# Optimization experiments

Measured on AMD Instinct MI355X. Metric: run time of the kernel, lower is better.

## Reference

```python
import jax, jax.numpy as jnp
import numpy as np

EPS = 1e-10


def setup_inputs() -> dict:
    key = jax.random.key(0)
    ks = jax.random.split(key, 8)
    b, s, m, r, n = 2, 2048, 1024, 64, 16
    u = jax.random.normal(ks[0], (b, s, m), dtype=jnp.float32)
    delta = jax.random.normal(ks[1], (b, s, r), dtype=jnp.float32)
    dt_proj_w = jax.random.normal(ks[2], (m, r), dtype=jnp.float32) * 0.02
    dt_proj_b = jax.random.normal(ks[3], (m,), dtype=jnp.float32) * 0.02
    # A_log ~ Uniform(-3, -1) as in nn.init.uniform_(self.A_log, -3.0, -1.0)
    A_log = jax.random.uniform(ks[4], (n, m), dtype=jnp.float32, minval=-3.0, maxval=-1.0)
    D_skip = jnp.ones((m,), dtype=jnp.float32)
    # xavier_uniform with gain=0.1 on [n, m]
    bound = 0.1 * np.sqrt(6.0 / (n + m))
    B_proj_w = jax.random.uniform(ks[5], (n, m), dtype=jnp.float32, minval=-bound, maxval=bound)
    C_proj_w = jax.random.uniform(ks[6], (n, m), dtype=jnp.float32, minval=-bound, maxval=bound)
    return {"u": u, "delta": delta, "dt_proj_w": dt_proj_w, "dt_proj_b": dt_proj_b,
            "A_log": A_log, "D_skip": D_skip, "B_proj_w": B_proj_w, "C_proj_w": C_proj_w}


def reference(u, delta, dt_proj_w, dt_proj_b, A_log, D_skip, B_proj_w, C_proj_w):
    # u: [b, s, m]; delta: [b, s, r]
    dt = jax.nn.softplus(jnp.einsum('bsr,mr->bsm', delta, dt_proj_w) + dt_proj_b)
    dt = jnp.clip(dt, 1e-6, 10.0)                      # [b, s, m]
    A = jnp.clip(-jnp.exp(A_log), -10.0, -1e-6)        # [n, m]
    B = jnp.einsum('bsm,nm->bsn', u, B_proj_w)         # [b, s, n]
    C = jnp.einsum('bsm,nm->bsn', u, C_proj_w)         # [b, s, n]

    # associative-scan path (seq_len > 256), math as in _associative_scan:
    # h_t = exp(cumsum_t log(dA)) * cumsum_t (dB_u / dA)
    dA = jnp.exp(dt[:, :, None, :] * A[None, None])    # [b, s, n, m]
    dA_c = jnp.clip(dA, EPS, None)
    dBu = dt[:, :, None, :] * B[..., None] * u[:, :, None, :]  # [b, s, n, m]
    A_cum = jnp.exp(jnp.cumsum(jnp.log(dA_c), axis=1))
    h = A_cum * jnp.cumsum(dBu / dA_c, axis=1)          # [b, s, n, m]
    y = jnp.einsum('bsnm,bsn->bsm', h, C)               # contract state dim

    out = y + u * D_skip
    out = jnp.clip(out, -10000.0, 10000.0)
    bad = jnp.any(~jnp.isfinite(out))
    return jnp.where(bad, jnp.zeros_like(u), out)
```

## Files before the change

kernel.cpp:

```cpp
#include <hip/hip_runtime.h>
#include <hip/hip_bf16.h>
#include <math.h>

#define B_ 2
#define S_ 2048
#define M_ 1024
#define R_ 64
#define N_ 16
#define NC 64
#define CH (S_/NC)

#define DT_OFF  0
#define P_OFF   4194304
#define H_OFF   6291456
#define BWT_OFF 8388608
#define CWT_OFF 8404992
#define PB_OFF  8421376
#define PC_OFF  8552448

__global__ __launch_bounds__(256) void k_dt(const float* __restrict__ delta,
                                            const float* __restrict__ Wdt,
                                            const float* __restrict__ bdt,
                                            const float* __restrict__ Bw,
                                            const float* __restrict__ Cw,
                                            float* __restrict__ dt,
                                            float* __restrict__ BwT,
                                            float* __restrict__ CwT) {
    int bid = blockIdx.y * 4 + blockIdx.x;
    if (threadIdx.x < 8) {
        int idx = bid * 8 + threadIdx.x;
        int mt = idx >> 4, nt = idx & 15;
        BwT[idx] = Bw[nt * M_ + mt];
        CwT[idx] = Cw[nt * M_ + mt];
    }
    int m    = blockIdx.x * 256 + threadIdx.x;
    int row0 = blockIdx.y * 8;
    float w[R_];
    const float4* W4 = reinterpret_cast<const float4*>(Wdt + (size_t)m * R_);
#pragma unroll
    for (int i = 0; i < R_ / 4; ++i) {
        float4 v = W4[i];
        w[4*i] = v.x; w[4*i+1] = v.y; w[4*i+2] = v.z; w[4*i+3] = v.w;
    }
    float bias = bdt[m];
#pragma unroll 1
    for (int r = 0; r < 8; ++r) {
        int bs = row0 + r;
        const float* dr = delta + (size_t)bs * R_;
        float acc = bias;
#pragma unroll
        for (int k = 0; k < R_; ++k) acc = fmaf(dr[k], w[k], acc);
        float sp = fmaxf(acc, 0.f) + log1pf(expf(-fabsf(acc)));
        sp = fminf(fmaxf(sp, 1e-6f), 10.0f);
        dt[(size_t)bs * M_ + m] = sp;
    }
}

__global__ __launch_bounds__(256) void k_bc_partial(const float* __restrict__ u,
                                                    const float* __restrict__ BwT,
                                                    const float* __restrict__ CwT,
                                                    float* __restrict__ pB,
                                                    float* __restrict__ pC) {
    __shared__ float uLds[16 * 516];
    int r0 = blockIdx.x * 16;
    int k0 = blockIdx.y * 512;
    for (int i = threadIdx.x; i < 2048; i += 256) {
        int r = i >> 7, kq = i & 127;
        float4 v = *reinterpret_cast<const float4*>(&u[(size_t)(r0 + r) * M_ + k0 + kq * 4]);
        *reinterpret_cast<float4*>(&uLds[r * 516 + kq * 4]) = v;
    }
    __syncthreads();
    int r = threadIdx.x >> 4, n = threadIdx.x & 15;
    const float4* u4 = reinterpret_cast<const float4*>(uLds + r * 516);
    float accB = 0.f, accC = 0.f;
#pragma unroll 4
    for (int k4 = 0; k4 < 128; ++k4) {
        float4 uv = u4[k4];
        int kb = k0 + k4 * 4;
        accB = fmaf(uv.x, BwT[(kb+0)*16 + n], accB);
        accB = fmaf(uv.y, BwT[(kb+1)*16 + n], accB);
        accB = fmaf(uv.z, BwT[(kb+2)*16 + n], accB);
        accB = fmaf(uv.w, BwT[(kb+3)*16 + n], accB);
        accC = fmaf(uv.x, CwT[(kb+0)*16 + n], accC);
        accC = fmaf(uv.y, CwT[(kb+1)*16 + n], accC);
        accC = fmaf(uv.z, CwT[(kb+2)*16 + n], accC);
        accC = fmaf(uv.w, CwT[(kb+3)*16 + n], accC);
    }
    size_t o = (size_t)blockIdx.y * 65536 + (size_t)(r0 + r) * 16 + n;
    pB[o] = accB;
    pC[o] = accC;
}

__global__ __launch_bounds__(256) void k_pass1(const float* __restrict__ dt,
                                               const float* __restrict__ u,
                                               const float* __restrict__ pB,
                                               const float* __restrict__ A_log,
                                               float* __restrict__ P,
                                               float* __restrict__ H) {
    __shared__ float ldsDt[CH * 64], ldsU[CH * 64], ldsB[CH * 16];
    int m0 = blockIdx.x * 64, c = blockIdx.y, b = blockIdx.z;
    int s0 = c * CH;
    int tid = threadIdx.x;
    for (int i = tid; i < 512; i += 256) {
        int s = i >> 4, mq = (i & 15) * 4;
        size_t off = ((size_t)(b * S_ + s0 + s)) * M_ + m0 + mq;
        *reinterpret_cast<float4*>(&ldsDt[s * 64 + mq]) = *reinterpret_cast<const float4*>(&dt[off]);
        *reinterpret_cast<float4*>(&ldsU [s * 64 + mq]) = *reinterpret_cast<const float4*>(&u[off]);
    }
    {
        size_t base = (size_t)(b * S_ + s0) * N_;
        for (int i = tid; i < CH * 16; i += 256)
            ldsB[i] = pB[base + i] + pB[65536 + base + i];
    }
    __syncthreads();
    int lane = tid & 63, wave = tid >> 6;
    int ml = wave * 16 + (lane & 15);
    int m  = m0 + ml;
    int n0 = (lane >> 4) * 4;
    float Aa[4], h[4] = {0,0,0,0}, g[4] = {1.f,1.f,1.f,1.f};
#pragma unroll
    for (int j = 0; j < 4; ++j) {
        float a = -expf(A_log[(size_t)(n0 + j) * M_ + m]);
        Aa[j] = fminf(fmaxf(a, -10.f), -1e-6f);
    }
    for (int s = 0; s < CH; ++s) {
        float dtv = ldsDt[s * 64 + ml];
        float uv  = ldsU [s * 64 + ml];
        float du  = dtv * uv;
        float4 bv = *reinterpret_cast<const float4*>(&ldsB[s * 16 + n0]);
        float bb[4] = {bv.x, bv.y, bv.z, bv.w};
#pragma unroll
        for (int j = 0; j < 4; ++j) {
            float ea = __expf(dtv * Aa[j]);
            h[j] = fmaf(ea, h[j], g[j] * (du * bb[j]));
            g[j] *= ea;
        }
    }
#pragma unroll
    for (int j = 0; j < 4; ++j) {
        size_t o = ((size_t)(b * 16 + n0 + j) * NC + c) * M_ + m;
        P[o] = g[j];
        H[o] = h[j];
    }
}

__global__ __launch_bounds__(64) void k_pass2(float* __restrict__ P,
                                              float* __restrict__ H) {
    int idx = blockIdx.x * 64 + threadIdx.x;
    int m = idx & (M_ - 1);
    int n = (idx >> 10) & 15;
    int b = idx >> 14;
    size_t base = ((size_t)(b * 16 + n) * NC) * M_ + m;
    float grun = 1.f, hrun = 0.f;
#pragma unroll 1
    for (int c0 = 0; c0 < NC; c0 += 8) {
        float pv[8], hv[8];
#pragma unroll
        for (int t = 0; t < 8; ++t) {
            pv[t] = P[base + (size_t)(c0 + t) * M_];
            hv[t] = H[base + (size_t)(c0 + t) * M_];
        }
#pragma unroll
        for (int t = 0; t < 8; ++t) {
            P[base + (size_t)(c0 + t) * M_] = grun;
            H[base + (size_t)(c0 + t) * M_] = hrun;
            hrun = fmaf(pv[t], hrun, grun * hv[t]);
            grun *= pv[t];
        }
    }
}

__global__ __launch_bounds__(256) void k_pass3(const float* __restrict__ dt,
                                               const float* __restrict__ u,
                                               const float* __restrict__ pB,
                                               const float* __restrict__ pC,
                                               const float* __restrict__ A_log,
                                               const float* __restrict__ Dskip,
                                               const float* __restrict__ Pinit,
                                               const float* __restrict__ Hinit,
                                               float* __restrict__ out) {
    __shared__ float ldsDt[CH * 64], ldsU[CH * 64], ldsB[CH * 16], ldsC[CH * 16];
    int m0 = blockIdx.x * 64, c = blockIdx.y, b = blockIdx.z;
    int s0 = c * CH;
    int tid = threadIdx.x;
    for (int i = tid; i < 512; i += 256) {
        int s = i >> 4, mq = (i & 15) * 4;
        size_t off = ((size_t)(b * S_ + s0 + s)) * M_ + m0 + mq;
        *reinterpret_cast<float4*>(&ldsDt[s * 64 + mq]) = *reinterpret_cast<const float4*>(&dt[off]);
        *reinterpret_cast<float4*>(&ldsU [s * 64 + mq]) = *reinterpret_cast<const float4*>(&u[off]);
    }
    {
        size_t base = (size_t)(b * S_ + s0) * N_;
        for (int i = tid; i < CH * 16; i += 256) {
            ldsB[i] = pB[base + i] + pB[65536 + base + i];
            ldsC[i] = pC[base + i] + pC[65536 + base + i];
        }
    }
    __syncthreads();
    int lane = tid & 63, wave = tid >> 6;
    int ml = wave * 16 + (lane & 15);
    int m  = m0 + ml;
    int ng = lane >> 4, n0 = ng * 4;
    float Aa[4], h[4], g[4];
#pragma unroll
    for (int j = 0; j < 4; ++j) {
        float a = -expf(A_log[(size_t)(n0 + j) * M_ + m]);
        Aa[j] = fminf(fmaxf(a, -10.f), -1e-6f);
        size_t o = ((size_t)(b * 16 + n0 + j) * NC + c) * M_ + m;
        g[j] = Pinit[o];
        h[j] = Hinit[o];
    }
    float Dm = Dskip[m];
    for (int s = 0; s < CH; ++s) {
        float dtv = ldsDt[s * 64 + ml];
        float uv  = ldsU [s * 64 + ml];
        float du  = dtv * uv;
        float4 bv = *reinterpret_cast<const float4*>(&ldsB[s * 16 + n0]);
        float4 cv = *reinterpret_cast<const float4*>(&ldsC[s * 16 + n0]);
        float bb[4] = {bv.x, bv.y, bv.z, bv.w};
        float cc[4] = {cv.x, cv.y, cv.z, cv.w};
        float y = 0.f;
#pragma unroll
        for (int j = 0; j < 4; ++j) {
            float ea = __expf(dtv * Aa[j]);
            h[j] = fmaf(ea, h[j], g[j] * (du * bb[j]));
            g[j] *= ea;
            y = fmaf(h[j], cc[j], y);
        }
        y += __shfl_xor(y, 16, 64);
        y += __shfl_xor(y, 32, 64);
        if (ng == 0) {
            float o = y + uv * Dm;
            o = fminf(fmaxf(o, -10000.f), 10000.f);
            out[((size_t)(b * S_ + s0 + s)) * M_ + m] = o;
        }
    }
}

extern "C" void kernel_launch(void* const* d_in, const int* in_sizes, int n_in,
                              void* d_out, int out_size, void* d_ws, size_t ws_size,
                              hipStream_t stream) {
    const float* u     = (const float*)d_in[0];
    const float* delta = (const float*)d_in[1];
    const float* Wdt   = (const float*)d_in[2];
    const float* bdt   = (const float*)d_in[3];
    const float* A_log = (const float*)d_in[4];
    const float* Dski  = (const float*)d_in[5];
    const float* Bw    = (const float*)d_in[6];
    const float* Cw    = (const float*)d_in[7];
    float* out = (float*)d_out;
    float* ws  = (float*)d_ws;

    float* dt  = ws + DT_OFF;
    float* P   = ws + P_OFF;
    float* H   = ws + H_OFF;
    float* BwT = ws + BWT_OFF;
    float* CwT = ws + CWT_OFF;
    float* pB  = ws + PB_OFF;
    float* pC  = ws + PC_OFF;

    k_dt<<<dim3(4, 512), 256, 0, stream>>>(delta, Wdt, bdt, Bw, Cw, dt, BwT, CwT);
    k_bc_partial<<<dim3(256, 2), 256, 0, stream>>>(u, BwT, CwT, pB, pC);
    k_pass1<<<dim3(16, NC, B_), 256, 0, stream>>>(dt, u, pB, A_log, P, H);
    k_pass2<<<512, 64, 0, stream>>>(P, H);
    k_pass3<<<dim3(16, NC, B_), 256, 0, stream>>>(dt, u, pB, pC, A_log, Dski, P, H, out);
}
```

Before: 106.8 us.

## Fuse all five stages into one cooperative kernel with grid syncs

Result: no change. 106.9 us (+0.1%).

```diff
diff --git a/kernel.cpp b/kernel.cpp
--- a/kernel.cpp
+++ b/kernel.cpp
@@ -1,6 +1,8 @@
 #include <hip/hip_runtime.h>
-#include <hip/hip_bf16.h>
+#include <hip/hip_cooperative_groups.h>
 #include <math.h>
+
+namespace cg = cooperative_groups;
 
 #define B_ 2
 #define S_ 2048
@@ -17,6 +19,247 @@
 #define CWT_OFF 8404992
 #define PB_OFF  8421376
 #define PC_OFF  8552448
+
+__global__ __launch_bounds__(256, 8) void k_mega(
+    const float* __restrict__ u, const float* __restrict__ delta,
+    const float* __restrict__ Wdt, const float* __restrict__ bdt,
+    const float* __restrict__ A_log, const float* __restrict__ Dskip,
+    const float* __restrict__ Bw, const float* __restrict__ Cw,
+    float* __restrict__ P, float* __restrict__ H,
+    float* __restrict__ Bp, float* __restrict__ Cp,
+    float* __restrict__ out)
+{
+    cg::grid_group grid = cg::this_grid();
+    __shared__ float lds[5120];
+    const int tid = threadIdx.x;
+    const int bid = blockIdx.x;
+    const int b   = bid >> 10;
+    const int c   = (bid >> 4) & 63;
+    const int m0  = (bid & 15) << 6;
+    const int s0  = c << 5;
+
+    if (bid < 512) {
+        const int msp = tid >> 4;
+        const int nn  = tid & 15;
+        const float4* wB4 = reinterpret_cast<const float4*>(Bw + (size_t)nn * M_ + msp * 64);
+        const float4* wC4 = reinterpret_cast<const float4*>(Cw + (size_t)nn * M_ + msp * 64);
+        for (int half = 0; half < 2; ++half) {
+            const int rowBase = bid * 8 + half * 4;
+            for (int i = tid; i < 1024; i += 256) {
+                int r = i >> 8, kq = i & 255;
+                *reinterpret_cast<float4*>(&lds[r * 1024 + kq * 4]) =
+                    *reinterpret_cast<const float4*>(&u[(size_t)(rowBase + r) * M_ + kq * 4]);
+            }
+            __syncthreads();
+            float accB[4] = {0.f,0.f,0.f,0.f}, accC[4] = {0.f,0.f,0.f,0.f};
+#pragma unroll 1
+            for (int k4 = 0; k4 < 16; ++k4) {
+                float4 wb = wB4[k4], wc = wC4[k4];
+#pragma unroll
+                for (int r = 0; r < 4; ++r) {
+                    float4 uv = *reinterpret_cast<const float4*>(&lds[r * 1024 + msp * 64 + k4 * 4]);
+                    accB[r] = fmaf(uv.x, wb.x, accB[r]);
+                    accB[r] = fmaf(uv.y, wb.y, accB[r]);
+                    accB[r] = fmaf(uv.z, wb.z, accB[r]);
+                    accB[r] = fmaf(uv.w, wb.w, accB[r]);
+                    accC[r] = fmaf(uv.x, wc.x, accC[r]);
+                    accC[r] = fmaf(uv.y, wc.y, accC[r]);
+                    accC[r] = fmaf(uv.z, wc.z, accC[r]);
+                    accC[r] = fmaf(uv.w, wc.w, accC[r]);
+                }
+            }
+#pragma unroll
+            for (int r = 0; r < 4; ++r) {
+                accB[r] += __shfl_xor(accB[r], 16, 64);
+                accB[r] += __shfl_xor(accB[r], 32, 64);
+                accC[r] += __shfl_xor(accC[r], 16, 64);
+                accC[r] += __shfl_xor(accC[r], 32, 64);
+            }
+            __syncthreads();
+            {
+                const int w  = tid >> 6;
+                const int ln = tid & 63;
+                if (ln < 16) {
+#pragma unroll
+                    for (int r = 0; r < 4; ++r) {
+                        lds[4096 + (w * 4 + r) * 16 + ln]       = accB[r];
+                        lds[4096 + 256 + (w * 4 + r) * 16 + ln] = accC[r];
+                    }
+                }
+            }
+            __syncthreads();
+            if (tid < 64) {
+                int r = tid >> 4, n2 = tid & 15;
+                float sB = 0.f, sC = 0.f;
+#pragma unroll
+                for (int w2 = 0; w2 < 4; ++w2) {
+                    sB += lds[4096 + (w2 * 4 + r) * 16 + n2];
+                    sC += lds[4096 + 256 + (w2 * 4 + r) * 16 + n2];
+                }
+                Bp[(size_t)(rowBase + r) * N_ + n2] = sB;
+                Cp[(size_t)(rowBase + r) * N_ + n2] = sC;
+            }
+            __syncthreads();
+        }
+    }
+
+    for (int i = tid; i < 512; i += 256) {
+        int s = i >> 4, kq = (i & 15) * 4;
+        *reinterpret_cast<float4*>(&lds[2048 + s * 64 + kq]) =
+            *reinterpret_cast<const float4*>(&delta[(size_t)(b * S_ + s0 + s) * R_ + kq]);
+    }
+    __syncthreads();
+    {
+        const int mlA = tid & 63;
+        const int sg  = tid >> 6;
+        const int mA  = m0 + mlA;
+        float bias = bdt[mA];
+        float acc[8];
+#pragma unroll
+        for (int i = 0; i < 8; ++i) acc[i] = bias;
+        const float4* W4 = reinterpret_cast<const float4*>(Wdt + (size_t)mA * R_);
+#pragma unroll 1
+        for (int kb = 0; kb < 8; ++kb) {
+            float4 w0 = W4[kb * 2], w1 = W4[kb * 2 + 1];
+#pragma unroll
+            for (int i = 0; i < 8; ++i) {
+                const float* dr = &lds[2048 + (sg * 8 + i) * 64 + kb * 8];
+                float4 d0 = *reinterpret_cast<const float4*>(dr);
+                float4 d1 = *reinterpret_cast<const float4*>(dr + 4);
+                acc[i] = fmaf(d0.x, w0.x, acc[i]);
+                acc[i] = fmaf(d0.y, w0.y, acc[i]);
+                acc[i] = fmaf(d0.z, w0.z, acc[i]);
+                acc[i] = fmaf(d0.w, w0.w, acc[i]);
+                acc[i] = fmaf(d1.x, w1.x, acc[i]);
+                acc[i] = fmaf(d1.y, w1.y, acc[i]);
+                acc[i] = fmaf(d1.z, w1.z, acc[i]);
+                acc[i] = fmaf(d1.w, w1.w, acc[i]);
+            }
+        }
+#pragma unroll
+        for (int i = 0; i < 8; ++i) {
+            float a2 = acc[i];
+            float sp = fmaxf(a2, 0.f) + log1pf(expf(-fabsf(a2)));
+            sp = fminf(fmaxf(sp, 1e-6f), 10.0f);
+            lds[(sg * 8 + i) * 64 + mlA] = sp;
+        }
+    }
+    __syncthreads();
+    for (int i = tid; i < 512; i += 256) {
+        int s = i >> 4, mq = (i & 15) * 4;
+        *reinterpret_cast<float4*>(&lds[2048 + s * 64 + mq]) =
+            *reinterpret_cast<const float4*>(&u[((size_t)(b * S_ + s0 + s)) * M_ + m0 + mq]);
+    }
+
+    const int lane = tid & 63;
+    const int wv   = tid >> 6;
+    const int ml   = wv * 16 + (lane & 15);
+    const int m    = m0 + ml;
+    const int ng   = lane >> 4;
+    const int n0   = ng * 4;
+    float Aa[4];
+#pragma unroll
+    for (int j = 0; j < 4; ++j) {
+        float a2 = -expf(A_log[(size_t)(n0 + j) * M_ + m]);
+        Aa[j] = fminf(fmaxf(a2, -10.f), -1e-6f);
+    }
+    const float Dm = Dskip[m];
+
+    grid.sync();
+
+    {
+        const size_t baseBC = (size_t)(b * S_ + s0) * N_;
+        if (tid < 128) {
+            *reinterpret_cast<float4*>(&lds[4096 + tid * 4]) =
+                *reinterpret_cast<const float4*>(&Bp[baseBC + tid * 4]);
+        } else {
+            *reinterpret_cast<float4*>(&lds[4608 + (tid - 128) * 4]) =
+                *reinterpret_cast<const float4*>(&Cp[baseBC + (tid - 128) * 4]);
+        }
+    }
+    __syncthreads();
+
+    float h[4] = {0.f,0.f,0.f,0.f}, g[4] = {1.f,1.f,1.f,1.f};
+    for (int s = 0; s < CH; ++s) {
+        float dtv = lds[s * 64 + ml];
+        float uv  = lds[2048 + s * 64 + ml];
+        float du  = dtv * uv;
+        float4 bv = *reinterpret_cast<const float4*>(&lds[4096 + s * 16 + n0]);
+        float bb[4] = {bv.x, bv.y, bv.z, bv.w};
+#pragma unroll
+        for (int j = 0; j < 4; ++j) {
+            float ea = __expf(dtv * Aa[j]);
+            h[j] = fmaf(ea, h[j], g[j] * (du * bb[j]));
+            g[j] *= ea;
+        }
+    }
+#pragma unroll
+    for (int j = 0; j < 4; ++j) {
+        size_t o = ((size_t)((b * N_ + n0 + j) * NC + c)) * M_ + m;
+        P[o] = g[j];
+        H[o] = h[j];
+    }
+
+    grid.sync();
+
+    if (bid < 128) {
+        const int idx = bid * 256 + tid;
+        const int mm  = idx & (M_ - 1);
+        const int nn2 = (idx >> 10) & 15;
+        const int bb2 = idx >> 14;
+        const size_t base2 = ((size_t)(bb2 * N_ + nn2) * NC) * M_ + mm;
+        float grun = 1.f, hrun = 0.f;
+#pragma unroll 1
+        for (int c0 = 0; c0 < NC; c0 += 8) {
+            float pv[8], hv[8];
+#pragma unroll
+            for (int t = 0; t < 8; ++t) {
+                pv[t] = P[base2 + (size_t)(c0 + t) * M_];
+                hv[t] = H[base2 + (size_t)(c0 + t) * M_];
+            }
+#pragma unroll
+            for (int t = 0; t < 8; ++t) {
+                P[base2 + (size_t)(c0 + t) * M_] = grun;
+                H[base2 + (size_t)(c0 + t) * M_] = hrun;
+                hrun = fmaf(pv[t], hrun, grun * hv[t]);
+                grun *= pv[t];
+            }
+        }
+    }
+
+    grid.sync();
+
+#pragma unroll
+    for (int j = 0; j < 4; ++j) {
+        size_t o = ((size_t)((b * N_ + n0 + j) * NC + c)) * M_ + m;
+        g[j] = P[o];
+        h[j] = H[o];
+    }
+    for (int s = 0; s < CH; ++s) {
+        float dtv = lds[s * 64 + ml];
+        float uv  = lds[2048 + s * 64 + ml];
+        float du  = dtv * uv;
+        float4 bv = *reinterpret_cast<const float4*>(&lds[4096 + s * 16 + n0]);
+        float4 cv = *reinterpret_cast<const float4*>(&lds[4608 + s * 16 + n0]);
+        float bb[4] = {bv.x, bv.y, bv.z, bv.w};
+        float cc[4] = {cv.x, cv.y, cv.z, cv.w};
+        float y = 0.f;
+#pragma unroll
+        for (int j = 0; j < 4; ++j) {
+            float ea = __expf(dtv * Aa[j]);
+            h[j] = fmaf(ea, h[j], g[j] * (du * bb[j]));
+            g[j] *= ea;
+            y = fmaf(h[j], cc[j], y);
+        }
+        y += __shfl_xor(y, 16, 64);
+        y += __shfl_xor(y, 32, 64);
+        if (ng == 0) {
+            float o2 = y + uv * Dm;
+            o2 = fminf(fmaxf(o2, -10000.f), 10000.f);
+            out[((size_t)(b * S_ + s0 + s)) * M_ + m] = o2;
+        }
+    }
+}
 
 __global__ __launch_bounds__(256) void k_dt(const float* __restrict__ delta,
                                             const float* __restrict__ Wdt,
@@ -259,6 +502,19 @@
     float* pB  = ws + PB_OFF;
     float* pC  = ws + PC_OFF;
 
+    int maxBlk = 0;
+    hipError_t qerr = hipOccupancyMaxActiveBlocksPerMultiprocessor(
+        &maxBlk, reinterpret_cast<const void*>(k_mega), 256, 0);
+    if (qerr == hipSuccess && maxBlk >= 8) {
+        void* args[] = {(void*)&u, (void*)&delta, (void*)&Wdt, (void*)&bdt,
+                        (void*)&A_log, (void*)&Dski, (void*)&Bw, (void*)&Cw,
+                        (void*)&P, (void*)&H, (void*)&pB, (void*)&pC, (void*)&out};
+        hipError_t lerr = hipLaunchCooperativeKernel(
+            reinterpret_cast<const void*>(k_mega), dim3(2048), dim3(256),
+            args, 0, stream);
+        if (lerr == hipSuccess) return;
+    }
+
     k_dt<<<dim3(4, 512), 256, 0, stream>>>(delta, Wdt, bdt, Bw, Cw, dt, BwT, CwT);
     k_bc_partial<<<dim3(256, 2), 256, 0, stream>>>(u, BwT, CwT, pB, pC);
     k_pass1<<<dim3(16, NC, B_), 256, 0, stream>>>(dt, u, pB, A_log, P, H);
```

## Merge front kernels, drop chunk-prefix kernel, recompute prefix in pass3

Applied to the files above, without the earlier changes.

Result: slower. 154.4 us (+44.6%).

```diff
diff --git a/kernel.cpp b/kernel.cpp
--- a/kernel.cpp
+++ b/kernel.cpp
@@ -1,5 +1,4 @@
 #include <hip/hip_runtime.h>
-#include <hip/hip_bf16.h>
 #include <math.h>
 
 #define B_ 2
@@ -7,101 +6,89 @@
 #define M_ 1024
 #define R_ 64
 #define N_ 16
-#define NC 64
-#define CH (S_/NC)
+#define NC 32
+#define CH 64
 
 #define DT_OFF  0
-#define P_OFF   4194304
-#define H_OFF   6291456
-#define BWT_OFF 8388608
-#define CWT_OFF 8404992
-#define PB_OFF  8421376
-#define PC_OFF  8552448
-
-__global__ __launch_bounds__(256) void k_dt(const float* __restrict__ delta,
-                                            const float* __restrict__ Wdt,
-                                            const float* __restrict__ bdt,
-                                            const float* __restrict__ Bw,
-                                            const float* __restrict__ Cw,
-                                            float* __restrict__ dt,
-                                            float* __restrict__ BwT,
-                                            float* __restrict__ CwT) {
-    int bid = blockIdx.y * 4 + blockIdx.x;
-    if (threadIdx.x < 8) {
-        int idx = bid * 8 + threadIdx.x;
-        int mt = idx >> 4, nt = idx & 15;
-        BwT[idx] = Bw[nt * M_ + mt];
-        CwT[idx] = Cw[nt * M_ + mt];
-    }
-    int m    = blockIdx.x * 256 + threadIdx.x;
-    int row0 = blockIdx.y * 8;
-    float w[R_];
-    const float4* W4 = reinterpret_cast<const float4*>(Wdt + (size_t)m * R_);
-#pragma unroll
-    for (int i = 0; i < R_ / 4; ++i) {
-        float4 v = W4[i];
-        w[4*i] = v.x; w[4*i+1] = v.y; w[4*i+2] = v.z; w[4*i+3] = v.w;
-    }
-    float bias = bdt[m];
+#define AGG_OFF 4194304
+#define PB_OFF  6291456
+#define PC_OFF  6422528
+
+__global__ __launch_bounds__(256) void k_front(
+    const float* __restrict__ u, const float* __restrict__ delta,
+    const float* __restrict__ Wdt, const float* __restrict__ bdt,
+    const float* __restrict__ Bw, const float* __restrict__ Cw,
+    float* __restrict__ dt, float* __restrict__ pB, float* __restrict__ pC)
+{
+    __shared__ float uLds[16 * 516];
+    const int bid = blockIdx.x;
+    const int tid = threadIdx.x;
+
+    if (bid < 512) {
+        const int r0 = (bid >> 1) * 16;
+        const int k0 = (bid & 1) * 512;
+        for (int i = tid; i < 2048; i += 256) {
+            int r = i >> 7, kq = i & 127;
+            *reinterpret_cast<float4*>(&uLds[r * 516 + kq * 4]) =
+                *reinterpret_cast<const float4*>(&u[(size_t)(r0 + r) * M_ + k0 + kq * 4]);
+        }
+        __syncthreads();
+        const int r = tid >> 4, n = tid & 15;
+        const float4* u4  = reinterpret_cast<const float4*>(uLds + r * 516);
+        const float4* wB4 = reinterpret_cast<const float4*>(Bw + (size_t)n * M_ + k0);
+        const float4* wC4 = reinterpret_cast<const float4*>(Cw + (size_t)n * M_ + k0);
+        float accB = 0.f, accC = 0.f;
+#pragma unroll 4
+        for (int k4 = 0; k4 < 128; ++k4) {
+            float4 uv = u4[k4], wb = wB4[k4], wc = wC4[k4];
+            accB = fmaf(uv.x, wb.x, accB);
+            accB = fmaf(uv.y, wb.y, accB);
+            accB = fmaf(uv.z, wb.z, accB);
+            accB = fmaf(uv.w, wb.w, accB);
+            accC = fmaf(uv.x, wc.x, accC);
+            accC = fmaf(uv.y, wc.y, accC);
+            accC = fmaf(uv.z, wc.z, accC);
+            accC = fmaf(uv.w, wc.w, accC);
+        }
+        size_t o = (size_t)(bid & 1) * 65536 + (size_t)(r0 + r) * 16 + n;
+        pB[o] = accB;
+        pC[o] = accC;
+    } else {
+        const int bid2 = bid - 512;
+        const int m    = (bid2 & 3) * 256 + tid;
+        const int row0 = (bid2 >> 2) * 8;
+        float w[R_];
+        const float4* W4 = reinterpret_cast<const float4*>(Wdt + (size_t)m * R_);
+#pragma unroll
+        for (int i = 0; i < R_ / 4; ++i) {
+            float4 v = W4[i];
+            w[4*i] = v.x; w[4*i+1] = v.y; w[4*i+2] = v.z; w[4*i+3] = v.w;
+        }
+        float bias = bdt[m];
 #pragma unroll 1
-    for (int r = 0; r < 8; ++r) {
-        int bs = row0 + r;
-        const float* dr = delta + (size_t)bs * R_;
-        float acc = bias;
-#pragma unroll
-        for (int k = 0; k < R_; ++k) acc = fmaf(dr[k], w[k], acc);
-        float sp = fmaxf(acc, 0.f) + log1pf(expf(-fabsf(acc)));
-        sp = fminf(fmaxf(sp, 1e-6f), 10.0f);
-        dt[(size_t)bs * M_ + m] = sp;
-    }
-}
-
-__global__ __launch_bounds__(256) void k_bc_partial(const float* __restrict__ u,
-                                                    const float* __restrict__ BwT,
-                                                    const float* __restrict__ CwT,
-                                                    float* __restrict__ pB,
-                                                    float* __restrict__ pC) {
-    __shared__ float uLds[16 * 516];
-    int r0 = blockIdx.x * 16;
-    int k0 = blockIdx.y * 512;
-    for (int i = threadIdx.x; i < 2048; i += 256) {
-        int r = i >> 7, kq = i & 127;
-        float4 v = *reinterpret_cast<const float4*>(&u[(size_t)(r0 + r) * M_ + k0 + kq * 4]);
-        *reinterpret_cast<float4*>(&uLds[r * 516 + kq * 4]) = v;
-    }
-    __syncthreads();
-    int r = threadIdx.x >> 4, n = threadIdx.x & 15;
-    const float4* u4 = reinterpret_cast<const float4*>(uLds + r * 516);
-    float accB = 0.f, accC = 0.f;
-#pragma unroll 4
-    for (int k4 = 0; k4 < 128; ++k4) {
-        float4 uv = u4[k4];
-        int kb = k0 + k4 * 4;
-        accB = fmaf(uv.x, BwT[(kb+0)*16 + n], accB);
-        accB = fmaf(uv.y, BwT[(kb+1)*16 + n], accB);
-        accB = fmaf(uv.z, BwT[(kb+2)*16 + n], accB);
-        accB = fmaf(uv.w, BwT[(kb+3)*16 + n], accB);
-        accC = fmaf(uv.x, CwT[(kb+0)*16 + n], accC);
-        accC = fmaf(uv.y, CwT[(kb+1)*16 + n], accC);
-        accC = fmaf(uv.z, CwT[(kb+2)*16 + n], accC);
-        accC = fmaf(uv.w, CwT[(kb+3)*16 + n], accC);
-    }
-    size_t o = (size_t)blockIdx.y * 65536 + (size_t)(r0 + r) * 16 + n;
-    pB[o] = accB;
-    pC[o] = accC;
+        for (int r = 0; r < 8; ++r) {
+            int bs = row0 + r;
+            const float* dr = delta + (size_t)bs * R_;
+            float acc = bias;
+#pragma unroll
+            for (int k = 0; k < R_; ++k) acc = fmaf(dr[k], w[k], acc);
+            float sp = fmaxf(acc, 0.f) + log1pf(expf(-fabsf(acc)));
+            sp = fminf(fmaxf(sp, 1e-6f), 10.0f);
+            dt[(size_t)bs * M_ + m] = sp;
+        }
+    }
 }
 
 __global__ __launch_bounds__(256) void k_pass1(const float* __restrict__ dt,
                                                const float* __restrict__ u,
                                                const float* __restrict__ pB,
                                                const float* __restrict__ A_log,
-                                               float* __restrict__ P,
-                                               float* __restrict__ H) {
+                                               float* __restrict__ Agg) {
     __shared__ float ldsDt[CH * 64], ldsU[CH * 64], ldsB[CH * 16];
-    int m0 = blockIdx.x * 64, c = blockIdx.y, b = blockIdx.z;
-    int s0 = c * CH;
-    int tid = threadIdx.x;
-    for (int i = tid; i < 512; i += 256) {
+    const int m0 = blockIdx.x * 64, c = blockIdx.y, b = blockIdx.z;
+    const int s0 = c * CH;
+    const int tid = threadIdx.x;
+    for (int i = tid; i < 1024; i += 256) {
         int s = i >> 4, mq = (i & 15) * 4;
         size_t off = ((size_t)(b * S_ + s0 + s)) * M_ + m0 + mq;
         *reinterpret_cast<float4*>(&ldsDt[s * 64 + mq]) = *reinterpret_cast<const float4*>(&dt[off]);
@@ -113,10 +100,10 @@
             ldsB[i] = pB[base + i] + pB[65536 + base + i];
     }
     __syncthreads();
-    int lane = tid & 63, wave = tid >> 6;
-    int ml = wave * 16 + (lane & 15);
-    int m  = m0 + ml;
-    int n0 = (lane >> 4) * 4;
+    const int lane = tid & 63, wave = tid >> 6;
+    const int ml = wave * 16 + (lane & 15);
+    const int m  = m0 + ml;
+    const int n0 = (lane >> 4) * 4;
     float Aa[4], h[4] = {0,0,0,0}, g[4] = {1.f,1.f,1.f,1.f};
 #pragma unroll
     for (int j = 0; j < 4; ++j) {
@@ -136,38 +123,11 @@
             g[j] *= ea;
         }
     }
-#pragma unroll
-    for (int j = 0; j < 4; ++j) {
-        size_t o = ((size_t)(b * 16 + n0 + j) * NC + c) * M_ + m;
-        P[o] = g[j];
-        H[o] = h[j];
-    }
-}
-
-__global__ __launch_bounds__(64) void k_pass2(float* __restrict__ P,
-                                              float* __restrict__ H) {
-    int idx = blockIdx.x * 64 + threadIdx.x;
-    int m = idx & (M_ - 1);
-    int n = (idx >> 10) & 15;
-    int b = idx >> 14;
-    size_t base = ((size_t)(b * 16 + n) * NC) * M_ + m;
-    float grun = 1.f, hrun = 0.f;
-#pragma unroll 1
-    for (int c0 = 0; c0 < NC; c0 += 8) {
-        float pv[8], hv[8];
-#pragma unroll
-        for (int t = 0; t < 8; ++t) {
-            pv[t] = P[base + (size_t)(c0 + t) * M_];
-            hv[t] = H[base + (size_t)(c0 + t) * M_];
-        }
-#pragma unroll
-        for (int t = 0; t < 8; ++t) {
-            P[base + (size_t)(c0 + t) * M_] = grun;
-            H[base + (size_t)(c0 + t) * M_] = hrun;
-            hrun = fmaf(pv[t], hrun, grun * hv[t]);
-            grun *= pv[t];
-        }
-    }
+    size_t base = ((size_t)(b * NC + c) * 1024 + m) * 32 + n0 * 2;
+    float4 w0 = make_float4(g[0], h[0], g[1], h[1]);
+    float4 w1 = make_float4(g[2], h[2], g[3], h[3]);
+    *reinterpret_cast<float4*>(&Agg[base])     = w0;
+    *reinterpret_cast<float4*>(&Agg[base + 4]) = w1;
 }
 
 __global__ __launch_bounds__(256) void k_pass3(const float* __restrict__ dt,
@@ -176,14 +136,13 @@
                                                const float* __restrict__ pC,
                                                const float* __restrict__ A_log,
                                                const float* __restrict__ Dskip,
-                                               const float* __restrict__ Pinit,
-                                               const float* __restrict__ Hinit,
+                                               const float* __restrict__ Agg,
                                                float* __restrict__ out) {
     __shared__ float ldsDt[CH * 64], ldsU[CH * 64], ldsB[CH * 16], ldsC[CH * 16];
-    int m0 = blockIdx.x * 64, c = blockIdx.y, b = blockIdx.z;
-    int s0 = c * CH;
-    int tid = threadIdx.x;
-    for (int i = tid; i < 512; i += 256) {
+    const int m0 = blockIdx.x * 64, c = blockIdx.y, b = blockIdx.z;
+    const int s0 = c * CH;
+    const int tid = threadIdx.x;
+    for (int i = tid; i < 1024; i += 256) {
         int s = i >> 4, mq = (i & 15) * 4;
         size_t off = ((size_t)(b * S_ + s0 + s)) * M_ + m0 + mq;
         *reinterpret_cast<float4*>(&ldsDt[s * 64 + mq]) = *reinterpret_cast<const float4*>(&dt[off]);
@@ -196,21 +155,33 @@
             ldsC[i] = pC[base + i] + pC[65536 + base + i];
         }
     }
-    __syncthreads();
-    int lane = tid & 63, wave = tid >> 6;
-    int ml = wave * 16 + (lane & 15);
-    int m  = m0 + ml;
-    int ng = lane >> 4, n0 = ng * 4;
-    float Aa[4], h[4], g[4];
+    const int lane = tid & 63, wave = tid >> 6;
+    const int ml = wave * 16 + (lane & 15);
+    const int m  = m0 + ml;
+    const int ng = lane >> 4, n0 = ng * 4;
+
+    float g[4] = {1.f,1.f,1.f,1.f}, h[4] = {0.f,0.f,0.f,0.f};
+    {
+        const float* aggP = Agg + ((size_t)(b * NC) * 1024 + m) * 32 + n0 * 2;
+#pragma unroll 1
+        for (int cp = 0; cp < c; ++cp) {
+            float4 a0 = *reinterpret_cast<const float4*>(aggP + (size_t)cp * 32768);
+            float4 a1 = *reinterpret_cast<const float4*>(aggP + (size_t)cp * 32768 + 4);
+            h[0] = fmaf(a0.x, h[0], g[0] * a0.y); g[0] *= a0.x;
+            h[1] = fmaf(a0.z, h[1], g[1] * a0.w); g[1] *= a0.z;
+            h[2] = fmaf(a1.x, h[2], g[2] * a1.y); g[2] *= a1.x;
+            h[3] = fmaf(a1.z, h[3], g[3] * a1.w); g[3] *= a1.z;
+        }
+    }
+    float Aa[4];
 #pragma unroll
     for (int j = 0; j < 4; ++j) {
         float a = -expf(A_log[(size_t)(n0 + j) * M_ + m]);
         Aa[j] = fminf(fmaxf(a, -10.f), -1e-6f);
-        size_t o = ((size_t)(b * 16 + n0 + j) * NC + c) * M_ + m;
-        g[j] = Pinit[o];
-        h[j] = Hinit[o];
-    }
-    float Dm = Dskip[m];
+    }
+    const float Dm = Dskip[m];
+    __syncthreads();
+
     for (int s = 0; s < CH; ++s) {
         float dtv = ldsDt[s * 64 + ml];
         float uv  = ldsU [s * 64 + ml];
@@ -252,16 +223,11 @@
     float* ws  = (float*)d_ws;
 
     float* dt  = ws + DT_OFF;
-    float* P   = ws + P_OFF;
-    float* H   = ws + H_OFF;
-    float* BwT = ws + BWT_OFF;
-    float* CwT = ws + CWT_OFF;
+    float* Agg = ws + AGG_OFF;
     float* pB  = ws + PB_OFF;
     float* pC  = ws + PC_OFF;
 
-    k_dt<<<dim3(4, 512), 256, 0, stream>>>(delta, Wdt, bdt, Bw, Cw, dt, BwT, CwT);
-    k_bc_partial<<<dim3(256, 2), 256, 0, stream>>>(u, BwT, CwT, pB, pC);
-    k_pass1<<<dim3(16, NC, B_), 256, 0, stream>>>(dt, u, pB, A_log, P, H);
-    k_pass2<<<512, 64, 0, stream>>>(P, H);
-    k_pass3<<<dim3(16, NC, B_), 256, 0, stream>>>(dt, u, pB, pC, A_log, Dski, P, H, out);
-}
+    k_front<<<2560, 256, 0, stream>>>(u, delta, Wdt, bdt, Bw, Cw, dt, pB, pC);
+    k_pass1<<<dim3(16, NC, B_), 256, 0, stream>>>(dt, u, pB, A_log, Agg);
+    k_pass3<<<dim3(16, NC, B_), 256, 0, stream>>>(dt, u, pB, pC, A_log, Dski, Agg, out);
+}
```
